# Performance work log

Hardware: AMD Instinct MI355X
Metric: run time of the kernel (lower is better)

Reference implementation:

```python
import jax, jax.numpy as jnp
import numpy as np

N_NODES = 100000


def gcn_conv(x, W, b, src, dst, n):
    # PyG GCNConv: linear transform, add self-loops, symmetric deg^{-1/2} norm, scatter-sum.
    h = x @ W  # [N, out]
    loop = jnp.arange(n, dtype=src.dtype)
    s = jnp.concatenate([src, loop])
    d = jnp.concatenate([dst, loop])
    deg = jax.ops.segment_sum(jnp.ones_like(d, dtype=h.dtype), d, num_segments=n)
    dinv = jnp.where(deg > 0, jax.lax.rsqrt(deg), 0.0)
    norm = dinv[s] * dinv[d]  # [E+N]
    msg = h[s] * norm[:, None]  # gather + scale
    out = jax.ops.segment_sum(msg, d, num_segments=n)  # scatter-add
    return out + b


def setup_inputs() -> dict:
    key = jax.random.key(0)
    ks = jax.random.split(key, 6)
    in_dim, hid, out_dim = 128, 128, 32
    n_edges = 1600000
    x = jax.random.normal(ks[0], (N_NODES, in_dim), dtype=jnp.float32)
    edge_index = jax.random.randint(ks[1], (2, n_edges), 0, N_NODES, dtype=jnp.int64)
    W1 = jax.random.normal(ks[2], (in_dim, hid), dtype=jnp.float32) / np.sqrt(in_dim)
    b1 = jnp.zeros((hid,), dtype=jnp.float32)
    W2 = jax.random.normal(ks[3], (hid, out_dim), dtype=jnp.float32) / np.sqrt(hid)
    b2 = jnp.zeros((out_dim,), dtype=jnp.float32)
    return {"x": x, "edge_index": edge_index, "W1": W1, "b1": b1, "W2": W2, "b2": b2}


def reference(x, edge_index, W1, b1, W2, b2):
    src, dst = edge_index[0], edge_index[1]
    h = gcn_conv(x, W1, b1, src, dst, N_NODES)
    h = jax.nn.relu(h)
    # F.dropout(training=False) in eval -> identity
    h = gcn_conv(h, W2, b2, src, dst, N_NODES)
    return jax.nn.log_softmax(h, axis=1)
```

## Files before the change

kernel.cpp:

```cpp
#include <hip/hip_runtime.h>
#include <hip/hip_bf16.h>
#include <math.h>

#define N_NODES 100000
#define N_EDGES 1600000
#define NB 196
#define CAP 16000
#define CHUNK 4096

typedef unsigned int uint;
typedef unsigned short ushort_t;
typedef unsigned char uchar_t;
typedef float f32x16 __attribute__((ext_vector_type(16)));
typedef float f32x2 __attribute__((ext_vector_type(2)));
typedef __bf16 bf16x8 __attribute__((ext_vector_type(8)));

__device__ __forceinline__ float bf2f(uint h) {
    union { uint u; float f; } x; x.u = h << 16; return x.f;
}
__device__ __forceinline__ unsigned short f2bf(float f) {
    union { float f; uint u; } x; x.f = f;
    uint u = x.u;
    return (unsigned short)((u + 0x7fffu + ((u >> 16) & 1u)) >> 16);
}
__device__ __forceinline__ uint pk2(float a, float b) {
    return (uint)f2bf(a) | ((uint)f2bf(b) << 16);
}
__device__ __forceinline__ bf16x8 bc8(uint4 u) { return __builtin_bit_cast(bf16x8, u); }

__device__ __forceinline__ int edge_at(const int* __restrict__ ei, int is32, long long idx) {
    return is32 ? ei[idx] : (int)(((const long long*)ei)[idx]);
}


__global__ __launch_bounds__(256) void k_bucket(const int* __restrict__ ei,
                                                const int* __restrict__ flag,
                                                int* __restrict__ cnt,
                                                uint* __restrict__ buf) {
    __shared__ uint stage[CHUNK];
    __shared__ unsigned char bid[CHUNK];
    __shared__ int lcnt[256], ls[256], lbase[256], gbase[256];
    int t = threadIdx.x;
    int is32 = *flag;
    lcnt[t] = 0;
    __syncthreads();
    int base = blockIdx.x * CHUNK;
    int srcv[16], dstv[16], offv[16];
    #pragma unroll
    for (int i = 0; i < 16; i++) {
        int e = base + i * 256 + t;
        if (e < N_EDGES) {
            srcv[i] = edge_at(ei, is32, e);
            dstv[i] = edge_at(ei, is32, (long long)N_EDGES + e);
            offv[i] = atomicAdd(&lcnt[dstv[i] >> 9], 1);
        } else {
            offv[i] = -1;
        }
    }
    __syncthreads();
    int c = lcnt[t];
    ls[t] = c;
    __syncthreads();
    int val = c;
    for (int off = 1; off < 256; off <<= 1) {
        int tmp = (t >= off) ? ls[t - off] : 0;
        __syncthreads();
        val += tmp;
        ls[t] = val;
        __syncthreads();
    }
    lbase[t] = val - c;
    if (c > 0) gbase[t] = atomicAdd(&cnt[t], c); else gbase[t] = 0;
    __syncthreads();
    int total = ls[255];
    #pragma unroll
    for (int i = 0; i < 16; i++) {
        if (offv[i] >= 0) {
            int b = dstv[i] >> 9;
            int p = lbase[b] + offv[i];
            stage[p] = (uint)srcv[i] | ((uint)(dstv[i] & 511) << 17);
            bid[p] = (unsigned char)b;
        }
    }
    __syncthreads();
    for (int idx = t; idx < total; idx += 256) {
        int b = bid[idx];
        int r = gbase[b] + (idx - lbase[b]);
        if (r < CAP) buf[(size_t)b * CAP + r] = stage[idx];
    }
}

__global__ __launch_bounds__(256) void k_build(const uint* __restrict__ buf,
                                               const int* __restrict__ cnt,
                                               int* __restrict__ row_start,
                                               float* __restrict__ dinv,
                                               int* __restrict__ csr_src) {
    __shared__ int ldeg[512], lexc[512], lcur[512], s[256];
    int t = threadIdx.x;
    int b = blockIdx.x;
    int cv = (t < NB) ? cnt[t] : 0;
    s[t] = cv;
    __syncthreads();
    int val = cv;
    for (int off = 1; off < 256; off <<= 1) {
        int tmp = (t >= off) ? s[t - off] : 0;
        __syncthreads();
        val += tmp;
        s[t] = val;
        __syncthreads();
    }
    int obase = (b == 0) ? 0 : s[b - 1];
    if (b == 0 && t == 0) row_start[N_NODES] = N_EDGES;
    int n0 = b << 9;
    int nn = min(512, N_NODES - n0);
    int ne = min(cnt[b], CAP);
    const uint* __restrict__ in = buf + (size_t)b * CAP;
    ldeg[t] = 0; ldeg[t + 256] = 0;
    lcur[t] = 0; lcur[t + 256] = 0;
    __syncthreads();
    for (int idx = t; idx < ne; idx += 256) {
        atomicAdd(&ldeg[in[idx] >> 17], 1);
    }
    __syncthreads();
    int v = ldeg[2 * t] + ldeg[2 * t + 1];
    s[t] = v;
    __syncthreads();
    int val2 = v;
    for (int off = 1; off < 256; off <<= 1) {
        int tmp = (t >= off) ? s[t - off] : 0;
        __syncthreads();
        val2 += tmp;
        s[t] = val2;
        __syncthreads();
    }
    int excl = val2 - v;
    lexc[2 * t] = excl;
    lexc[2 * t + 1] = excl + ldeg[2 * t];
    __syncthreads();
    for (int i = t; i < nn; i += 256) {
        row_start[n0 + i] = obase + lexc[i];
        dinv[n0 + i] = rsqrtf((float)(ldeg[i] + 1));
    }
    __syncthreads();
    for (int idx = t; idx < ne; idx += 256) {
        uint p = in[idx];
        int dl = p >> 17;
        int pos = obase + lexc[dl] + atomicAdd(&lcur[dl], 1);
        csr_src[pos] = (int)(p & 0x1FFFFu);
    }
}

__global__ void k_prep(const float* __restrict__ W1, const float* __restrict__ W2,
                       ushort_t* __restrict__ wt1, ushort_t* __restrict__ w2t,
                       const int* __restrict__ ei, int* __restrict__ flag) {
    int t = threadIdx.x;
    if (blockIdx.x == 0) {
        int v = ei[2 * t + 1] | ei[2 * (t + 256) + 1];
        if (v) atomicOr(flag, 1);
    }
    int i = blockIdx.x * 256 + t;
    if (i < 16384) {
        int c = i >> 7, k = i & 127;
        wt1[i] = f2bf(W1[k * 128 + c]);
    } else if (i < 20480) {
        int j = i - 16384;
        int c = j >> 7, p = j & 127;
        int cl = (p & 3) * 32 + (p >> 2);
        w2t[j] = f2bf(W2[cl * 32 + c]);
    }
}

__global__ __launch_bounds__(256) void k_gemm1(const float4* __restrict__ xf,
                                               const uint4* __restrict__ wt1,
                                               const float* __restrict__ dinv,
                                               uint* __restrict__ g1p) {
    __shared__ uint4 WT[128 * 16];
    int t = threadIdx.x;
    #pragma unroll
    for (int i = 0; i < 8; i++) {
        int gi = i * 256 + t;
        int c = gi >> 4, g = gi & 15;
        WT[c * 16 + (g ^ (c & 15))] = wt1[gi];
    }
    __syncthreads();
    int w = t >> 6, l = t & 63;
    int row0 = blockIdx.x * 128 + w * 32;
    int crow = min(row0 + (l & 31), N_NODES - 1);
    int hi = l >> 5;
    f32x16 acc[4];
    #pragma unroll
    for (int ct = 0; ct < 4; ct++)
        #pragma unroll
        for (int r = 0; r < 16; r++) acc[ct][r] = 0.0f;
    const float4* ap = xf + (size_t)crow * 32;
    #pragma unroll
    for (int k0 = 0; k0 < 8; k0++) {
        float4 f0 = ap[(k0 * 2 + hi) * 2];
        float4 f1 = ap[(k0 * 2 + hi) * 2 + 1];
        uint4 au;
        au.x = pk2(f0.x, f0.y); au.y = pk2(f0.z, f0.w);
        au.z = pk2(f1.x, f1.y); au.w = pk2(f1.z, f1.w);
        bf16x8 a = bc8(au);
        #pragma unroll
        for (int ct = 0; ct < 4; ct++) {
            int col = ct * 32 + (l & 31);
            bf16x8 b = bc8(WT[col * 16 + ((k0 * 2 + hi) ^ (col & 15))]);
            acc[ct] = __builtin_amdgcn_mfma_f32_32x32x16_bf16(a, b, acc[ct], 0, 0, 0);
        }
    }
    #pragma unroll
    for (int reg = 0; reg < 16; reg++) {
        int row = row0 + (reg & 3) + 8 * (reg >> 2) + 4 * hi;
        if (row < N_NODES) {
            float d = dinv[row];
            int pw = __builtin_amdgcn_cvt_pk_fp8_f32(acc[0][reg] * d, acc[1][reg] * d, 0, false);
            pw = __builtin_amdgcn_cvt_pk_fp8_f32(acc[2][reg] * d, acc[3][reg] * d, pw, true);
            g1p[(size_t)row * 32 + (l & 31)] = (uint)pw;
        }
    }
}

__global__ __launch_bounds__(256) void k_agg1(const uint2* __restrict__ g1p2,
                                              const float* __restrict__ dinv,
                                              const float* __restrict__ b1,
                                              const int* __restrict__ row_start,
                                              const int* __restrict__ csr_src,
                                              uint4* __restrict__ a1) {
    int v = blockIdx.x * 16 + (threadIdx.x >> 4);
    int L = threadIdx.x & 15;
    float s0, s1, s2, s3, s4, s5, s6, s7;
    {
        uint2 u = g1p2[(size_t)v * 16 + L];
        f32x2 a0 = __builtin_amdgcn_cvt_pk_f32_fp8(u.x, false);
        f32x2 a1f = __builtin_amdgcn_cvt_pk_f32_fp8(u.x, true);
        f32x2 a2 = __builtin_amdgcn_cvt_pk_f32_fp8(u.y, false);
        f32x2 a3 = __builtin_amdgcn_cvt_pk_f32_fp8(u.y, true);
        s0 = a0[0]; s1 = a0[1]; s2 = a1f[0]; s3 = a1f[1];
        s4 = a2[0]; s5 = a2[1]; s6 = a3[0]; s7 = a3[1];
    }
    int jb = row_start[v], je = row_start[v + 1];
    int j = jb;
    for (; j + 16 <= je; j += 16) {
        int idx[16];
        #pragma unroll
        for (int q = 0; q < 16; q++) idx[q] = csr_src[j + q];
        uint2 d[16];
        #pragma unroll
        for (int q = 0; q < 16; q++) d[q] = g1p2[(size_t)idx[q] * 16 + L];
        #pragma unroll
        for (int q = 0; q < 16; q++) {
            f32x2 a0 = __builtin_amdgcn_cvt_pk_f32_fp8(d[q].x, false);
            f32x2 a1f = __builtin_amdgcn_cvt_pk_f32_fp8(d[q].x, true);
            f32x2 a2 = __builtin_amdgcn_cvt_pk_f32_fp8(d[q].y, false);
            f32x2 a3 = __builtin_amdgcn_cvt_pk_f32_fp8(d[q].y, true);
            s0 += a0[0]; s1 += a0[1]; s2 += a1f[0]; s3 += a1f[1];
            s4 += a2[0]; s5 += a2[1]; s6 += a3[0]; s7 += a3[1];
        }
    }
    for (; j + 4 <= je; j += 4) {
        int idx[4];
        #pragma unroll
        for (int q = 0; q < 4; q++) idx[q] = csr_src[j + q];
        uint2 d[4];
        #pragma unroll
        for (int q = 0; q < 4; q++) d[q] = g1p2[(size_t)idx[q] * 16 + L];
        #pragma unroll
        for (int q = 0; q < 4; q++) {
            f32x2 a0 = __builtin_amdgcn_cvt_pk_f32_fp8(d[q].x, false);
            f32x2 a1f = __builtin_amdgcn_cvt_pk_f32_fp8(d[q].x, true);
            f32x2 a2 = __builtin_amdgcn_cvt_pk_f32_fp8(d[q].y, false);
            f32x2 a3 = __builtin_amdgcn_cvt_pk_f32_fp8(d[q].y, true);
            s0 += a0[0]; s1 += a0[1]; s2 += a1f[0]; s3 += a1f[1];
            s4 += a2[0]; s5 += a2[1]; s6 += a3[0]; s7 += a3[1];
        }
    }
    for (; j < je; j++) {
        uint2 u = g1p2[(size_t)csr_src[j] * 16 + L];
        f32x2 a0 = __builtin_amdgcn_cvt_pk_f32_fp8(u.x, false);
        f32x2 a1f = __builtin_amdgcn_cvt_pk_f32_fp8(u.x, true);
        f32x2 a2 = __builtin_amdgcn_cvt_pk_f32_fp8(u.y, false);
        f32x2 a3 = __builtin_amdgcn_cvt_pk_f32_fp8(u.y, true);
        s0 += a0[0]; s1 += a0[1]; s2 += a1f[0]; s3 += a1f[1];
        s4 += a2[0]; s5 += a2[1]; s6 += a3[0]; s7 += a3[1];
    }
    float d = dinv[v];
    int c0 = 2 * L;
    float o0 = fmaxf(d * s0 + b1[c0], 0.0f);
    float o1 = fmaxf(d * s1 + b1[32 + c0], 0.0f);
    float o2 = fmaxf(d * s2 + b1[64 + c0], 0.0f);
    float o3 = fmaxf(d * s3 + b1[96 + c0], 0.0f);
    float o4 = fmaxf(d * s4 + b1[c0 + 1], 0.0f);
    float o5 = fmaxf(d * s5 + b1[32 + c0 + 1], 0.0f);
    float o6 = fmaxf(d * s6 + b1[64 + c0 + 1], 0.0f);
    float o7 = fmaxf(d * s7 + b1[96 + c0 + 1], 0.0f);
    uint4 ow;
    ow.x = pk2(o0, o1); ow.y = pk2(o2, o3);
    ow.z = pk2(o4, o5); ow.w = pk2(o6, o7);
    a1[(size_t)v * 16 + L] = ow;
}

__global__ __launch_bounds__(256) void k_gemm2(const uint4* __restrict__ a1v,
                                               const uint4* __restrict__ w2t,
                                               const float* __restrict__ dinv,
                                               uchar_t* __restrict__ g2p) {
    __shared__ uint4 WT[32 * 16];
    int t = threadIdx.x;
    #pragma unroll
    for (int i = 0; i < 2; i++) {
        int gi = i * 256 + t;
        int c = gi >> 4, g = gi & 15;
        WT[c * 16 + (g ^ (c & 15))] = w2t[gi];
    }
    __syncthreads();
    int w = t >> 6, l = t & 63;
    int row0 = blockIdx.x * 128 + w * 32;
    int crow = min(row0 + (l & 31), N_NODES - 1);
    int hi = l >> 5;
    int col = l & 31;
    f32x16 acc;
    #pragma unroll
    for (int r = 0; r < 16; r++) acc[r] = 0.0f;
    const uint4* ap = a1v + (size_t)crow * 16;
    #pragma unroll
    for (int k0 = 0; k0 < 8; k0++) {
        bf16x8 a = bc8(ap[k0 * 2 + hi]);
        bf16x8 b = bc8(WT[col * 16 + ((k0 * 2 + hi) ^ (col & 15))]);
        acc = __builtin_amdgcn_mfma_f32_32x32x16_bf16(a, b, acc, 0, 0, 0);
    }
    #pragma unroll
    for (int reg = 0; reg < 16; reg++) {
        int row = row0 + (reg & 3) + 8 * (reg >> 2) + 4 * hi;
        if (row < N_NODES) {
            float z = acc[reg] * dinv[row];
            int pw = __builtin_amdgcn_cvt_pk_fp8_f32(z, z, 0, false);
            g2p[(size_t)row * 32 + col] = (uchar_t)(pw & 0xff);
        }
    }
}

__global__ __launch_bounds__(256) void k_agg2(const uint* __restrict__ g2p4,
                                              const float* __restrict__ dinv,
                                              const float* __restrict__ b2,
                                              const int* __restrict__ row_start,
                                              const int* __restrict__ csr_src,
                                              float4* __restrict__ out) {
    int v = blockIdx.x * 32 + (threadIdx.x >> 3);
    int L = threadIdx.x & 7;
    float s0, s1, s2, s3;
    {
        uint u = g2p4[(size_t)v * 8 + L];
        f32x2 a0 = __builtin_amdgcn_cvt_pk_f32_fp8(u, false);
        f32x2 a1f = __builtin_amdgcn_cvt_pk_f32_fp8(u, true);
        s0 = a0[0]; s1 = a0[1]; s2 = a1f[0]; s3 = a1f[1];
    }
    int jb = row_start[v], je = row_start[v + 1];
    int j = jb;
    for (; j + 8 <= je; j += 8) {
        int i0 = csr_src[j + 0], i1 = csr_src[j + 1];
        int i2 = csr_src[j + 2], i3 = csr_src[j + 3];
        int i4 = csr_src[j + 4], i5 = csr_src[j + 5];
        int i6 = csr_src[j + 6], i7 = csr_src[j + 7];
        uint d0 = g2p4[(size_t)i0 * 8 + L];
        uint d1 = g2p4[(size_t)i1 * 8 + L];
        uint d2 = g2p4[(size_t)i2 * 8 + L];
        uint d3 = g2p4[(size_t)i3 * 8 + L];
        uint d4 = g2p4[(size_t)i4 * 8 + L];
        uint d5 = g2p4[(size_t)i5 * 8 + L];
        uint d6 = g2p4[(size_t)i6 * 8 + L];
        uint d7 = g2p4[(size_t)i7 * 8 + L];
        #pragma unroll
        for (int q = 0; q < 8; q++) {
            uint uu = q == 0 ? d0 : q == 1 ? d1 : q == 2 ? d2 : q == 3 ? d3
                    : q == 4 ? d4 : q == 5 ? d5 : q == 6 ? d6 : d7;
            f32x2 a0 = __builtin_amdgcn_cvt_pk_f32_fp8(uu, false);
            f32x2 a1f = __builtin_amdgcn_cvt_pk_f32_fp8(uu, true);
            s0 += a0[0]; s1 += a0[1]; s2 += a1f[0]; s3 += a1f[1];
        }
    }
    for (; j < je; j++) {
        uint u = g2p4[(size_t)csr_src[j] * 8 + L];
        f32x2 a0 = __builtin_amdgcn_cvt_pk_f32_fp8(u, false);
        f32x2 a1f = __builtin_amdgcn_cvt_pk_f32_fp8(u, true);
        s0 += a0[0]; s1 += a0[1]; s2 += a1f[0]; s3 += a1f[1];
    }
    float dv = dinv[v];
    int c0 = 4 * L;
    float z0 = dv * s0 + b2[c0];
    float z1 = dv * s1 + b2[c0 + 1];
    float z2 = dv * s2 + b2[c0 + 2];
    float z3 = dv * s3 + b2[c0 + 3];
    float m = fmaxf(fmaxf(z0, z1), fmaxf(z2, z3));
    #pragma unroll
    for (int off = 4; off >= 1; off >>= 1) m = fmaxf(m, __shfl_xor(m, off));
    float e = __expf(z0 - m) + __expf(z1 - m) + __expf(z2 - m) + __expf(z3 - m);
    #pragma unroll
    for (int off = 4; off >= 1; off >>= 1) e += __shfl_xor(e, off);
    float lg = __logf(e);
    float4 o;
    o.x = (z0 - m) - lg;
    o.y = (z1 - m) - lg;
    o.z = (z2 - m) - lg;
    o.w = (z3 - m) - lg;
    out[(size_t)v * 8 + L] = o;
}


extern "C" void kernel_launch(void* const* d_in, const int* in_sizes, int n_in,
                              void* d_out, int out_size, void* d_ws, size_t ws_size,
                              hipStream_t stream) {
    const float* x  = (const float*)d_in[0];
    const int*   ei = (const int*)d_in[1];
    const float* W1 = (const float*)d_in[2];
    const float* b1 = (const float*)d_in[3];
    const float* W2 = (const float*)d_in[4];
    const float* b2 = (const float*)d_in[5];
    float* out = (float*)d_out;

    char* ws = (char*)d_ws;
    size_t off = 0;
    auto alloc = [&](size_t bytes) {
        void* p = ws + off;
        off = (off + bytes + 255) & ~255ULL;
        return p;
    };
    int* flag = (int*)alloc(4);
    int* cnt  = (int*)alloc((size_t)NB * 4);
    size_t zero_bytes = off;
    int*   row_start = (int*)alloc((size_t)(N_NODES + 1) * 4);
    float* dinv      = (float*)alloc((size_t)N_NODES * 4);
    int*   csr_src   = (int*)alloc((size_t)N_EDGES * 4);
    ushort_t* wt1g   = (ushort_t*)alloc(16384 * 2);
    ushort_t* w2tg   = (ushort_t*)alloc(4096 * 2);
    uint*  g1p       = (uint*)alloc((size_t)N_NODES * 128);
    void* uregion = alloc((size_t)N_NODES * 128 * 2);
    uint*  buf = (uint*)uregion;
    uint4* a1  = (uint4*)uregion;
    uchar_t* g2p = (uchar_t*)g1p;

    hipMemsetAsync(flag, 0, zero_bytes, stream);

    k_prep<<<80, 256, 0, stream>>>(W1, W2, wt1g, w2tg, ei, flag);
    k_bucket<<<(N_EDGES + CHUNK - 1) / CHUNK, 256, 0, stream>>>(ei, flag, cnt, buf);
    k_build<<<NB, 256, 0, stream>>>(buf, cnt, row_start, dinv, csr_src);
    k_gemm1<<<(N_NODES + 127) / 128, 256, 0, stream>>>((const float4*)x, (const uint4*)wt1g, dinv, g1p);
    k_agg1<<<N_NODES / 16, 256, 0, stream>>>((const uint2*)g1p, dinv, b1, row_start, csr_src, a1);
    k_gemm2<<<(N_NODES + 127) / 128, 256, 0, stream>>>((const uint4*)a1, (const uint4*)w2tg, dinv, g2p);
    k_agg2<<<N_NODES / 32, 256, 0, stream>>>((const uint*)g2p, dinv, b2, row_start, csr_src, (float4*)out);
}
```

Before: 147.1 us.

## Split layer-1 aggregation into four feature slices and enlarge bucket chunks

The layer-1 aggregation now runs as four separate feature slices of 32 bytes each per node instead of one pass over all 128 bytes. Each slice's gather working set (100k nodes x 32 bytes) is smaller and may stay cache resident, so random neighbor gathers hit cache more often. The output is stored slice-major and the second GEMM reads its A operand from that layout. The edge bucketing kernel also doubles its chunk size and runs 512 threads per block, halving the number of blocks and global atomics. The cost is re-reading row_start and the CSR indices four times, plus narrower 4-byte gathers per lane.

After: 197.3 us. 1.34x slower.

```diff
diff --git a/kernel.cpp b/kernel.cpp
--- a/kernel.cpp
+++ b/kernel.cpp
@@ -6,7 +6,7 @@
 #define N_EDGES 1600000
 #define NB 196
 #define CAP 16000
-#define CHUNK 4096
+#define CHUNK 8192
 
 typedef unsigned int uint;
 typedef unsigned short ushort_t;
@@ -33,7 +33,7 @@
 }
 
 
-__global__ __launch_bounds__(256) void k_bucket(const int* __restrict__ ei,
+__global__ __launch_bounds__(512) void k_bucket(const int* __restrict__ ei,
                                                 const int* __restrict__ flag,
                                                 int* __restrict__ cnt,
                                                 uint* __restrict__ buf) {
@@ -42,13 +42,13 @@
     __shared__ int lcnt[256], ls[256], lbase[256], gbase[256];
     int t = threadIdx.x;
     int is32 = *flag;
-    lcnt[t] = 0;
+    if (t < 256) lcnt[t] = 0;
     __syncthreads();
     int base = blockIdx.x * CHUNK;
     int srcv[16], dstv[16], offv[16];
     #pragma unroll
     for (int i = 0; i < 16; i++) {
-        int e = base + i * 256 + t;
+        int e = base + i * 512 + t;
         if (e < N_EDGES) {
             srcv[i] = edge_at(ei, is32, e);
             dstv[i] = edge_at(ei, is32, (long long)N_EDGES + e);
@@ -58,19 +58,20 @@
         }
     }
     __syncthreads();
-    int c = lcnt[t];
-    ls[t] = c;
+    int c = 0;
+    if (t < 256) { c = lcnt[t]; ls[t] = c; }
     __syncthreads();
     int val = c;
     for (int off = 1; off < 256; off <<= 1) {
-        int tmp = (t >= off) ? ls[t - off] : 0;
-        __syncthreads();
-        val += tmp;
-        ls[t] = val;
-        __syncthreads();
-    }
-    lbase[t] = val - c;
-    if (c > 0) gbase[t] = atomicAdd(&cnt[t], c); else gbase[t] = 0;
+        int tmp = (t >= off && t < 256) ? ls[t - off] : 0;
+        __syncthreads();
+        if (t < 256) { val += tmp; ls[t] = val; }
+        __syncthreads();
+    }
+    if (t < 256) {
+        lbase[t] = val - c;
+        gbase[t] = (c > 0) ? atomicAdd(&cnt[t], c) : 0;
+    }
     __syncthreads();
     int total = ls[255];
     #pragma unroll
@@ -83,7 +84,7 @@
         }
     }
     __syncthreads();
-    for (int idx = t; idx < total; idx += 256) {
+    for (int idx = t; idx < total; idx += 512) {
         int b = bid[idx];
         int r = gbase[b] + (idx - lbase[b]);
         if (r < CAP) buf[(size_t)b * CAP + r] = stage[idx];
@@ -220,23 +221,22 @@
     }
 }
 
-__global__ __launch_bounds__(256) void k_agg1(const uint2* __restrict__ g1p2,
+__global__ __launch_bounds__(256) void k_agg1(const uint* __restrict__ g1p,
                                               const float* __restrict__ dinv,
                                               const float* __restrict__ b1,
                                               const int* __restrict__ row_start,
                                               const int* __restrict__ csr_src,
-                                              uint4* __restrict__ a1) {
-    int v = blockIdx.x * 16 + (threadIdx.x >> 4);
-    int L = threadIdx.x & 15;
-    float s0, s1, s2, s3, s4, s5, s6, s7;
+                                              uint2* __restrict__ a1s) {
+    int s = blockIdx.x & 3;
+    int v = (blockIdx.x >> 2) * 32 + (threadIdx.x >> 3);
+    int a = threadIdx.x & 7;
+    const uint* __restrict__ g = g1p + 8 * s + a;
+    float s0, s1, s2, s3;
     {
-        uint2 u = g1p2[(size_t)v * 16 + L];
-        f32x2 a0 = __builtin_amdgcn_cvt_pk_f32_fp8(u.x, false);
-        f32x2 a1f = __builtin_amdgcn_cvt_pk_f32_fp8(u.x, true);
-        f32x2 a2 = __builtin_amdgcn_cvt_pk_f32_fp8(u.y, false);
-        f32x2 a3 = __builtin_amdgcn_cvt_pk_f32_fp8(u.y, true);
-        s0 = a0[0]; s1 = a0[1]; s2 = a1f[0]; s3 = a1f[1];
-        s4 = a2[0]; s5 = a2[1]; s6 = a3[0]; s7 = a3[1];
+        uint u = g[(size_t)v * 32];
+        f32x2 lo = __builtin_amdgcn_cvt_pk_f32_fp8(u, false);
+        f32x2 hh = __builtin_amdgcn_cvt_pk_f32_fp8(u, true);
+        s0 = lo[0]; s1 = lo[1]; s2 = hh[0]; s3 = hh[1];
     }
     int jb = row_start[v], je = row_start[v + 1];
     int j = jb;
@@ -244,59 +244,46 @@
         int idx[16];
         #pragma unroll
         for (int q = 0; q < 16; q++) idx[q] = csr_src[j + q];
-        uint2 d[16];
-        #pragma unroll
-        for (int q = 0; q < 16; q++) d[q] = g1p2[(size_t)idx[q] * 16 + L];
+        uint d[16];
+        #pragma unroll
+        for (int q = 0; q < 16; q++) d[q] = g[(size_t)idx[q] * 32];
         #pragma unroll
         for (int q = 0; q < 16; q++) {
-            f32x2 a0 = __builtin_amdgcn_cvt_pk_f32_fp8(d[q].x, false);
-            f32x2 a1f = __builtin_amdgcn_cvt_pk_f32_fp8(d[q].x, true);
-            f32x2 a2 = __builtin_amdgcn_cvt_pk_f32_fp8(d[q].y, false);
-            f32x2 a3 = __builtin_amdgcn_cvt_pk_f32_fp8(d[q].y, true);
-            s0 += a0[0]; s1 += a0[1]; s2 += a1f[0]; s3 += a1f[1];
-            s4 += a2[0]; s5 += a2[1]; s6 += a3[0]; s7 += a3[1];
+            f32x2 lo = __builtin_amdgcn_cvt_pk_f32_fp8(d[q], false);
+            f32x2 hh = __builtin_amdgcn_cvt_pk_f32_fp8(d[q], true);
+            s0 += lo[0]; s1 += lo[1]; s2 += hh[0]; s3 += hh[1];
         }
     }
     for (; j + 4 <= je; j += 4) {
         int idx[4];
         #pragma unroll
         for (int q = 0; q < 4; q++) idx[q] = csr_src[j + q];
-        uint2 d[4];
-        #pragma unroll
-        for (int q = 0; q < 4; q++) d[q] = g1p2[(size_t)idx[q] * 16 + L];
+        uint d[4];
+        #pragma unroll
+        for (int q = 0; q < 4; q++) d[q] = g[(size_t)idx[q] * 32];
         #pragma unroll
         for (int q = 0; q < 4; q++) {
-            f32x2 a0 = __builtin_amdgcn_cvt_pk_f32_fp8(d[q].x, false);
-            f32x2 a1f = __builtin_amdgcn_cvt_pk_f32_fp8(d[q].x, true);
-            f32x2 a2 = __builtin_amdgcn_cvt_pk_f32_fp8(d[q].y, false);
-            f32x2 a3 = __builtin_amdgcn_cvt_pk_f32_fp8(d[q].y, true);
-            s0 += a0[0]; s1 += a0[1]; s2 += a1f[0]; s3 += a1f[1];
-            s4 += a2[0]; s5 += a2[1]; s6 += a3[0]; s7 += a3[1];
+            f32x2 lo = __builtin_amdgcn_cvt_pk_f32_fp8(d[q], false);
+            f32x2 hh = __builtin_amdgcn_cvt_pk_f32_fp8(d[q], true);
+            s0 += lo[0]; s1 += lo[1]; s2 += hh[0]; s3 += hh[1];
         }
     }
     for (; j < je; j++) {
-        uint2 u = g1p2[(size_t)csr_src[j] * 16 + L];
-        f32x2 a0 = __builtin_amdgcn_cvt_pk_f32_fp8(u.x, false);
-        f32x2 a1f = __builtin_amdgcn_cvt_pk_f32_fp8(u.x, true);
-        f32x2 a2 = __builtin_amdgcn_cvt_pk_f32_fp8(u.y, false);
-        f32x2 a3 = __builtin_amdgcn_cvt_pk_f32_fp8(u.y, true);
-        s0 += a0[0]; s1 += a0[1]; s2 += a1f[0]; s3 += a1f[1];
-        s4 += a2[0]; s5 += a2[1]; s6 += a3[0]; s7 += a3[1];
+        uint u = g[(size_t)csr_src[j] * 32];
+        f32x2 lo = __builtin_amdgcn_cvt_pk_f32_fp8(u, false);
+        f32x2 hh = __builtin_amdgcn_cvt_pk_f32_fp8(u, true);
+        s0 += lo[0]; s1 += lo[1]; s2 += hh[0]; s3 += hh[1];
     }
     float d = dinv[v];
-    int c0 = 2 * L;
-    float o0 = fmaxf(d * s0 + b1[c0], 0.0f);
-    float o1 = fmaxf(d * s1 + b1[32 + c0], 0.0f);
-    float o2 = fmaxf(d * s2 + b1[64 + c0], 0.0f);
-    float o3 = fmaxf(d * s3 + b1[96 + c0], 0.0f);
-    float o4 = fmaxf(d * s4 + b1[c0 + 1], 0.0f);
-    float o5 = fmaxf(d * s5 + b1[32 + c0 + 1], 0.0f);
-    float o6 = fmaxf(d * s6 + b1[64 + c0 + 1], 0.0f);
-    float o7 = fmaxf(d * s7 + b1[96 + c0 + 1], 0.0f);
-    uint4 ow;
-    ow.x = pk2(o0, o1); ow.y = pk2(o2, o3);
-    ow.z = pk2(o4, o5); ow.w = pk2(o6, o7);
-    a1[(size_t)v * 16 + L] = ow;
+    int cb = 8 * s + 2 * (a >> 1) + (a & 1);
+    float o0 = fmaxf(d * s0 + b1[cb], 0.0f);
+    float o1 = fmaxf(d * s1 + b1[32 + cb], 0.0f);
+    float o2 = fmaxf(d * s2 + b1[64 + cb], 0.0f);
+    float o3 = fmaxf(d * s3 + b1[96 + cb], 0.0f);
+    uint2 ow;
+    ow.x = pk2(o0, o1);
+    ow.y = pk2(o2, o3);
+    a1s[((size_t)s * N_NODES + v) * 8 + a] = ow;
 }
 
 __global__ __launch_bounds__(256) void k_gemm2(const uint4* __restrict__ a1v,
@@ -320,11 +307,11 @@
     f32x16 acc;
     #pragma unroll
     for (int r = 0; r < 16; r++) acc[r] = 0.0f;
-    const uint4* ap = a1v + (size_t)crow * 16;
     #pragma unroll
     for (int k0 = 0; k0 < 8; k0++) {
-        bf16x8 a = bc8(ap[k0 * 2 + hi]);
-        bf16x8 b = bc8(WT[col * 16 + ((k0 * 2 + hi) ^ (col & 15))]);
+        int g = k0 * 2 + hi;
+        bf16x8 a = bc8(a1v[((size_t)(g >> 2) * N_NODES + crow) * 4 + (g & 3)]);
+        bf16x8 b = bc8(WT[col * 16 + (g ^ (col & 15))]);
         acc = __builtin_amdgcn_mfma_f32_32x32x16_bf16(a, b, acc, 0, 0, 0);
     }
     #pragma unroll
@@ -433,17 +420,17 @@
     ushort_t* w2tg   = (ushort_t*)alloc(4096 * 2);
     uint*  g1p       = (uint*)alloc((size_t)N_NODES * 128);
     void* uregion = alloc((size_t)N_NODES * 128 * 2);
-    uint*  buf = (uint*)uregion;
-    uint4* a1  = (uint4*)uregion;
+    uint*  buf  = (uint*)uregion;
+    uint2* a1s  = (uint2*)uregion;
     uchar_t* g2p = (uchar_t*)g1p;
 
     hipMemsetAsync(flag, 0, zero_bytes, stream);
 
     k_prep<<<80, 256, 0, stream>>>(W1, W2, wt1g, w2tg, ei, flag);
-    k_bucket<<<(N_EDGES + CHUNK - 1) / CHUNK, 256, 0, stream>>>(ei, flag, cnt, buf);
+    k_bucket<<<(N_EDGES + CHUNK - 1) / CHUNK, 512, 0, stream>>>(ei, flag, cnt, buf);
     k_build<<<NB, 256, 0, stream>>>(buf, cnt, row_start, dinv, csr_src);
     k_gemm1<<<(N_NODES + 127) / 128, 256, 0, stream>>>((const float4*)x, (const uint4*)wt1g, dinv, g1p);
-    k_agg1<<<N_NODES / 16, 256, 0, stream>>>((const uint2*)g1p, dinv, b1, row_start, csr_src, a1);
-    k_gemm2<<<(N_NODES + 127) / 128, 256, 0, stream>>>((const uint4*)a1, (const uint4*)w2tg, dinv, g2p);
+    k_agg1<<<4 * (N_NODES / 32), 256, 0, stream>>>(g1p, dinv, b1, row_start, csr_src, a1s);
+    k_gemm2<<<(N_NODES + 127) / 128, 256, 0, stream>>>((const uint4*)a1s, (const uint4*)w2tg, dinv, g2p);
     k_agg2<<<N_NODES / 32, 256, 0, stream>>>((const uint*)g2p, dinv, b2, row_start, csr_src, (float4*)out);
 }
```
